# Performance work log

Measured on AMD Instinct MI355X. Metric: run time of the kernel, lower is better.

The kernel has to match this reference:

```python
import jax, jax.numpy as jnp
import numpy as np

B, L, D_MODEL, H = 2, 2048, 1024, 16
D_HEAD = D_MODEL // H
NEG = -1e9


def setup_inputs() -> dict:
    key = jax.random.key(0)
    ks = jax.random.split(key, 8)
    q = jax.random.normal(ks[0], (B, L, D_MODEL), dtype=jnp.float32)
    k = jax.random.normal(ks[1], (B, L, D_MODEL), dtype=jnp.float32)
    v = jax.random.normal(ks[2], (B, L, D_MODEL), dtype=jnp.float32)
    # causal mask: True where attention is disallowed (masked_fill semantics)
    mask = jnp.broadcast_to(jnp.triu(jnp.ones((L, L), dtype=bool), k=1), (B, L, L))
    s = 1.0 / np.sqrt(D_MODEL)
    Wq = jax.random.normal(ks[3], (D_MODEL, D_MODEL), dtype=jnp.float32) * s
    Wk = jax.random.normal(ks[4], (D_MODEL, D_MODEL), dtype=jnp.float32) * s
    Wv = jax.random.normal(ks[5], (D_MODEL, D_MODEL), dtype=jnp.float32) * s
    Wo = jax.random.normal(ks[6], (D_MODEL, D_MODEL), dtype=jnp.float32) * s
    return {"q": q, "k": k, "v": v, "mask": mask,
            "Wq": Wq, "Wk": Wk, "Wv": Wv, "Wo": Wo}


def reference(q, k, v, mask, Wq, Wk, Wv, Wo):
    # projections (Linear, bias=False)
    qh = (q @ Wq).reshape(B, L, H, D_HEAD)
    kh = (k @ Wk).reshape(B, L, H, D_HEAD)
    vh = (v @ Wv).reshape(B, L, H, D_HEAD)
    # per-head scores: contiguous d_model slices == head reshape
    scores = jnp.einsum("bqhd,bkhd->bhqk", qh, kh)
    scores = jnp.where(mask[:, None, :, :], NEG, scores)
    # NOTE: original applies softmax FIRST, then divides by sqrt(d_head)
    weights = jax.nn.softmax(scores, axis=-1) / np.sqrt(D_HEAD).astype(np.float32)
    att = jnp.einsum("bhqk,bkhd->bqhd", weights, vh).reshape(B, L, D_MODEL)
    # dropout is identity in eval mode
    return att @ Wo
```

## Files before the change

kernel.cpp:

```cpp
#include <hip/hip_runtime.h>
#include <hip/hip_bf16.h>

#define BATCH  2
#define SEQ    2048
#define DMODEL 1024
#define NHEAD  16
#define DHEAD  64

typedef _Float16 f16x4 __attribute__((ext_vector_type(4)));
typedef _Float16 f16x8 __attribute__((ext_vector_type(8)));
typedef float    f32x4 __attribute__((ext_vector_type(4)));

union H16 { unsigned short u; _Float16 f; };
__device__ __forceinline__ _Float16 u2h(unsigned short u) { H16 c; c.u = u; return c.f; }
__device__ __forceinline__ unsigned short h2u(_Float16 f) { H16 c; c.f = f; return c.u; }

__device__ __forceinline__ void gll16(const void* g, void* l) {
    __builtin_amdgcn_global_load_lds(
        (const __attribute__((address_space(1))) void*)g,
        (__attribute__((address_space(3))) void*)l, 16, 0, 0);
}

__device__ __forceinline__ void pack_body(const float* __restrict__ W,
                                          _Float16* __restrict__ Phi,
                                          _Float16* __restrict__ Plo)
{
    const int n0 = blockIdx.x * 64;
    const int k0 = blockIdx.y * 64;
    const int t  = threadIdx.x;
    const int nl = t & 63;
    const int kc = (t >> 6) * 16;
    const int n  = n0 + nl;
    const int sw = (n & 3) ^ ((n >> 2) & 3);

    _Float16 hi[16], lo[16];
#pragma unroll
    for (int i = 0; i < 16; i++) {
        float x = W[(size_t)(k0 + kc + i) * DMODEL + n] * 32.0f;
        _Float16 h = (_Float16)x;
        hi[i] = h;
        lo[i] = (_Float16)(x - (float)h);
    }
#pragma unroll
    for (int cc = 0; cc < 2; cc++) {
        const int kk = kc + cc * 8;
        const int g  = kk >> 5;
        const int c  = (kk >> 3) & 3;
        const size_t off = (size_t)n * DMODEL + k0 + g * 32 + ((c ^ sw) << 3);
        *(f16x8*)&Phi[off] = *(f16x8*)&hi[cc * 8];
        if (Plo) *(f16x8*)&Plo[off] = *(f16x8*)&lo[cc * 8];
    }
}

__global__ __launch_bounds__(256) void pack_qkv(const float* __restrict__ Wq,
                                                const float* __restrict__ Wk,
                                                const float* __restrict__ Wv,
                                                _Float16* qhiT, _Float16* qloT,
                                                _Float16* khiT, _Float16* kloT,
                                                _Float16* vhiT)
{
    const int z = blockIdx.z;
    pack_body(z == 0 ? Wq : z == 1 ? Wk : Wv,
              z == 0 ? qhiT : z == 1 ? khiT : vhiT,
              z == 0 ? qloT : z == 1 ? kloT : nullptr);
}

__global__ __launch_bounds__(256) void pack_one(const float* __restrict__ W,
                                                _Float16* Phi)
{
    pack_body(W, Phi, nullptr);
}

template <int SPLIT, typename CT>
__global__ __launch_bounds__(256) void gemm_mfma(const float* __restrict__ A0,
                                                 const float* __restrict__ A1,
                                                 const _Float16* __restrict__ Bh0,
                                                 const _Float16* __restrict__ Bl0,
                                                 const _Float16* __restrict__ Bh1,
                                                 const _Float16* __restrict__ Bl1,
                                                 CT* __restrict__ C0,
                                                 CT* __restrict__ C1,
                                                 int N, int K)
{
    constexpr int ASZ = 128 * 40;
    constexpr int BSZ = 128 * 32;
    constexpr int AHI = 0;
    constexpr int ALO = ASZ;
    constexpr int BHI = ASZ * (SPLIT == 3 ? 2 : 1);
    constexpr int BLO = BHI + 2 * BSZ;
    constexpr int TOT = BHI + 2 * BSZ * (SPLIT == 3 ? 2 : 1);
    __shared__ __align__(16) _Float16 smem[TOT];

    const float*    A  = blockIdx.z ? A1 : A0;
    const _Float16* Bh = blockIdx.z ? Bh1 : Bh0;
    const _Float16* Bl = blockIdx.z ? Bl1 : Bl0;
    CT*             C  = blockIdx.z ? C1 : C0;

    const int m0 = blockIdx.x * 128;
    const int n0 = blockIdx.y * 128;
    const int t    = threadIdx.x;
    const int wave = t >> 6;
    const int lane = t & 63;
    const int quad = lane >> 4;
    const int col  = lane & 15;
    const int wm   = (wave & 1) * 64;
    const int wn   = (wave >> 1) * 64;

    const int ar  = t >> 1;
    const int akc = (t & 1) * 16;
    const float* Ap = A + (size_t)(m0 + ar) * K + akc;

    const _Float16* BhSrc = Bh + (size_t)(n0 + wave * 32 + (lane >> 2)) * K + (lane & 3) * 8;
    const _Float16* BlSrc = (SPLIT == 3)
        ? Bl + (size_t)(n0 + wave * 32 + (lane >> 2)) * K + (lane & 3) * 8 : nullptr;

    const int qe8 = (quad ^ ((col & 3) ^ ((col >> 2) & 3))) * 8;

    f32x4 acc[4][4];
#pragma unroll
    for (int mt = 0; mt < 4; mt++)
#pragma unroll
        for (int nt = 0; nt < 4; nt++) acc[mt][nt] = (f32x4){0.f, 0.f, 0.f, 0.f};

    float av[16];
    auto loadA = [&](int k0) {
#pragma unroll
        for (int g = 0; g < 4; g++) {
            float4 x = *(const float4*)(Ap + k0 + g * 4);
            av[g * 4 + 0] = x.x; av[g * 4 + 1] = x.y;
            av[g * 4 + 2] = x.z; av[g * 4 + 3] = x.w;
        }
    };
    auto issueB = [&](int k0, int buf) {
        _Float16* d0 = &smem[BHI + buf * BSZ + wave * 1024];
        gll16(BhSrc + k0, d0);
        gll16(BhSrc + (size_t)16 * K + k0, d0 + 512);
        if constexpr (SPLIT == 3) {
            _Float16* d1 = &smem[BLO + buf * BSZ + wave * 1024];
            gll16(BlSrc + k0, d1);
            gll16(BlSrc + (size_t)16 * K + k0, d1 + 512);
        }
    };
    auto storeA = [&]() {
#pragma unroll
        for (int g = 0; g < 2; g++) {
            f16x8 h, l;
#pragma unroll
            for (int j = 0; j < 8; j++) {
                float x = av[g * 8 + j];
                _Float16 hh = (_Float16)x;
                h[j] = hh;
                l[j] = (_Float16)(x - (float)hh);
            }
            *(f16x8*)&smem[AHI + ar * 40 + akc + g * 8] = h;
            if constexpr (SPLIT == 3)
                *(f16x8*)&smem[ALO + ar * 40 + akc + g * 8] = l;
        }
    };

    loadA(0);
    issueB(0, 0);

    int buf = 0;
    for (int k0 = 0; k0 < K; k0 += 32, buf ^= 1) {
        storeA();
        __syncthreads();

        if (k0 + 32 < K) { issueB(k0 + 32, buf ^ 1); loadA(k0 + 32); }

        f16x8 ah[4], al[4], bh[4], bl[4];
#pragma unroll
        for (int mt = 0; mt < 4; mt++) {
            ah[mt] = *(f16x8*)&smem[AHI + (wm + mt * 16 + col) * 40 + quad * 8];
            if constexpr (SPLIT == 3)
                al[mt] = *(f16x8*)&smem[ALO + (wm + mt * 16 + col) * 40 + quad * 8];
        }
#pragma unroll
        for (int nt = 0; nt < 4; nt++) {
            bh[nt] = *(f16x8*)&smem[BHI + buf * BSZ + (wn + nt * 16 + col) * 32 + qe8];
            if constexpr (SPLIT == 3)
                bl[nt] = *(f16x8*)&smem[BLO + buf * BSZ + (wn + nt * 16 + col) * 32 + qe8];
        }
#pragma unroll
        for (int nt = 0; nt < 4; nt++)
#pragma unroll
            for (int mt = 0; mt < 4; mt++) {
                acc[mt][nt] = __builtin_amdgcn_mfma_f32_16x16x32_f16(ah[mt], bh[nt], acc[mt][nt], 0, 0, 0);
                if constexpr (SPLIT == 3) {
                    acc[mt][nt] = __builtin_amdgcn_mfma_f32_16x16x32_f16(ah[mt], bl[nt], acc[mt][nt], 0, 0, 0);
                    acc[mt][nt] = __builtin_amdgcn_mfma_f32_16x16x32_f16(al[mt], bh[nt], acc[mt][nt], 0, 0, 0);
                }
            }
        __syncthreads();
    }

    const float inv = 1.0f / 32.0f;
#pragma unroll
    for (int mt = 0; mt < 4; mt++)
#pragma unroll
        for (int nt = 0; nt < 4; nt++)
#pragma unroll
            for (int r = 0; r < 4; r++) {
                float val = acc[mt][nt][r] * inv;
                size_t idx = (size_t)(m0 + wm + mt * 16 + quad * 4 + r) * N
                           + n0 + wn + nt * 16 + col;
                if constexpr (SPLIT == 3) {
                    _Float16 h = (_Float16)val;
                    _Float16 l = (_Float16)(val - (float)h);
                    C[idx] = (unsigned)h2u(h) | ((unsigned)h2u(l) << 16);
                } else if constexpr (__is_same(CT, _Float16)) {
                    C[idx] = (_Float16)val;
                } else {
                    C[idx] = val;
                }
            }
}

#define LDS_STRIDE 72
#define KHI_OFF 0
#define KLO_OFF (64 * LDS_STRIDE)
#define VT_OFF  (2 * 64 * LDS_STRIDE)
#define VT_SIZE (64 * LDS_STRIDE + 64)
#define P_OFF   (VT_OFF + VT_SIZE)
#define P_WAVE  (16 * LDS_STRIDE)
#define SMEM_HALVES (P_OFF + 4 * P_WAVE)

__global__ __launch_bounds__(256) void attn_mfma(unsigned* __restrict__ qa,
                                                 const unsigned* __restrict__ kh,
                                                 const _Float16* __restrict__ vh)
{
    __shared__ __align__(16) _Float16 smem[SMEM_HALVES];

    const int i  = blockIdx.x;
    const int j  = i >> 3;
    const int bh = (i & 7) + ((j & 3) << 3);
    const int qt = (SEQ / 64 - 1) - (j >> 2);
    const int b  = bh >> 4;
    const int h  = bh & 15;
    const int qb = qt * 64;

    const int t    = threadIdx.x;
    const int wave = t >> 6;
    const int lane = t & 63;
    const int quad = lane >> 4;
    const int col  = lane & 15;

    const size_t bbase = (size_t)b * SEQ * DMODEL + (size_t)h * DHEAD;
    const unsigned* kb_ptr = kh + bbase;
    const _Float16* vb_ptr = vh + bbase;

    const int qm = qb + wave * 16 + col;
    f16x8 qhi[2], qlo[2];
    {
        const unsigned* qp = qa + bbase + (size_t)qm * DMODEL + quad * 8;
#pragma unroll
        for (int kt = 0; kt < 2; kt++) {
            uint4 u0 = *(const uint4*)(qp + kt * 32);
            uint4 u1 = *(const uint4*)(qp + kt * 32 + 4);
            unsigned us[8] = {u0.x, u0.y, u0.z, u0.w, u1.x, u1.y, u1.z, u1.w};
#pragma unroll
            for (int jj = 0; jj < 8; jj++) {
                qhi[kt][jj] = u2h((unsigned short)(us[jj] & 0xffffu));
                qlo[kt][jj] = u2h((unsigned short)(us[jj] >> 16));
            }
        }
    }

    const int srow = t >> 2;
    const int sdg  = (t & 3) << 4;
    const int vswz = (t & 3) * 16;

    f16x8 kOnes;
#pragma unroll
    for (int jj = 0; jj < 8; jj++) kOnes[jj] = (_Float16)1.0f;

    float m_i[4];
    f32x4 l4 = (f32x4){0.f, 0.f, 0.f, 0.f};
    f32x4 o[4];
#pragma unroll
    for (int r = 0; r < 4; r++) m_i[r] = -1e30f;
#pragma unroll
    for (int dt = 0; dt < 4; dt++) o[dt] = (f32x4){0.f, 0.f, 0.f, 0.f};

    const int wq0 = qb + wave * 16;
    _Float16* Pw = &smem[P_OFF + wave * P_WAVE];

    f16x8 pkhi[2], pklo[2], pv[2];
    auto load_tile = [&](int kb) {
        const unsigned* kp = kb_ptr + (size_t)(kb + srow) * DMODEL + sdg;
        uint4 u0 = *(const uint4*)(kp + 0);
        uint4 u1 = *(const uint4*)(kp + 4);
        uint4 u2 = *(const uint4*)(kp + 8);
        uint4 u3 = *(const uint4*)(kp + 12);
        unsigned us[16] = {u0.x, u0.y, u0.z, u0.w, u1.x, u1.y, u1.z, u1.w,
                           u2.x, u2.y, u2.z, u2.w, u3.x, u3.y, u3.z, u3.w};
#pragma unroll
        for (int g = 0; g < 2; g++)
#pragma unroll
            for (int jj = 0; jj < 8; jj++) {
                pkhi[g][jj] = u2h((unsigned short)(us[g * 8 + jj] & 0xffffu));
                pklo[g][jj] = u2h((unsigned short)(us[g * 8 + jj] >> 16));
            }
        const _Float16* vp = vb_ptr + (size_t)(kb + srow) * DMODEL + sdg;
        pv[0] = *(const f16x8*)vp;
        pv[1] = *(const f16x8*)(vp + 8);
    };

    load_tile(0);

    for (int kb = 0; kb <= qb; kb += 64) {
        __syncthreads();

        *(f16x8*)&smem[KHI_OFF + srow * LDS_STRIDE + sdg]     = pkhi[0];
        *(f16x8*)&smem[KHI_OFF + srow * LDS_STRIDE + sdg + 8] = pkhi[1];
        *(f16x8*)&smem[KLO_OFF + srow * LDS_STRIDE + sdg]     = pklo[0];
        *(f16x8*)&smem[KLO_OFF + srow * LDS_STRIDE + sdg + 8] = pklo[1];
#pragma unroll
        for (int jj = 0; jj < 8; jj++) {
            smem[VT_OFF + (sdg + jj    ) * LDS_STRIDE + vswz + srow] = pv[0][jj];
            smem[VT_OFF + (sdg + 8 + jj) * LDS_STRIDE + vswz + srow] = pv[1][jj];
        }
        __syncthreads();

        if (kb + 64 <= qb) load_tile(kb + 64);

        if (kb > wq0 + 15) continue;

        f32x4 acc[4];
#pragma unroll
        for (int ct = 0; ct < 4; ct++) acc[ct] = (f32x4){0.f, 0.f, 0.f, 0.f};
#pragma unroll
        for (int kt = 0; kt < 2; kt++) {
#pragma unroll
            for (int ct = 0; ct < 4; ct++) {
                f16x8 bhi = *(f16x8*)&smem[KHI_OFF + (ct * 16 + col) * LDS_STRIDE + kt * 32 + quad * 8];
                f16x8 blo = *(f16x8*)&smem[KLO_OFF + (ct * 16 + col) * LDS_STRIDE + kt * 32 + quad * 8];
                acc[ct] = __builtin_amdgcn_mfma_f32_16x16x32_f16(qhi[kt], bhi, acc[ct], 0, 0, 0);
                acc[ct] = __builtin_amdgcn_mfma_f32_16x16x32_f16(qhi[kt], blo, acc[ct], 0, 0, 0);
                acc[ct] = __builtin_amdgcn_mfma_f32_16x16x32_f16(qlo[kt], bhi, acc[ct], 0, 0, 0);
            }
        }

        const bool need_mask = (kb + 63 > wq0);
#pragma unroll
        for (int r = 0; r < 4; r++) {
            const int qrow = wq0 + quad * 4 + r;
            float s0 = acc[0][r], s1 = acc[1][r], s2 = acc[2][r], s3 = acc[3][r];
            if (need_mask) {
                s0 = (kb +  0 + col <= qrow) ? s0 : -1e30f;
                s1 = (kb + 16 + col <= qrow) ? s1 : -1e30f;
                s2 = (kb + 32 + col <= qrow) ? s2 : -1e30f;
                s3 = (kb + 48 + col <= qrow) ? s3 : -1e30f;
            }
            float rm = fmaxf(fmaxf(s0, s1), fmaxf(s2, s3));
#pragma unroll
            for (int off = 1; off <= 8; off <<= 1)
                rm = fmaxf(rm, __shfl_xor(rm, off, 64));
            const float mnew  = fmaxf(m_i[r], rm);
            const float alpha = __expf(m_i[r] - mnew);
            const float p0 = __expf(s0 - mnew), p1 = __expf(s1 - mnew);
            const float p2 = __expf(s2 - mnew), p3 = __expf(s3 - mnew);
            m_i[r] = mnew;
            l4[r] *= alpha;
#pragma unroll
            for (int dt = 0; dt < 4; dt++) o[dt][r] *= alpha;
            const int prow = quad * 4 + r;
            Pw[prow * LDS_STRIDE + col     ] = (_Float16)p0;
            Pw[prow * LDS_STRIDE + col + 16] = (_Float16)p1;
            Pw[prow * LDS_STRIDE + col + 32] = (_Float16)p2;
            Pw[prow * LDS_STRIDE + col + 48] = (_Float16)p3;
        }

#pragma unroll
        for (int kt = 0; kt < 2; kt++) {
            f16x8 a = *(f16x8*)&Pw[col * LDS_STRIDE + kt * 32 + quad * 8];
            l4 = __builtin_amdgcn_mfma_f32_16x16x32_f16(a, kOnes, l4, 0, 0, 0);
#pragma unroll
            for (int dt = 0; dt < 4; dt++) {
                f16x8 bv = *(f16x8*)&smem[VT_OFF + (dt * 16 + col) * LDS_STRIDE + (dt & 3) * 16 + kt * 32 + quad * 8];
                o[dt] = __builtin_amdgcn_mfma_f32_16x16x32_f16(a, bv, o[dt], 0, 0, 0);
            }
        }
    }

#pragma unroll
    for (int r = 0; r < 4; r++) {
        const float inv = 1.0f / (l4[r] * 8.0f);
        const int q = wq0 + quad * 4 + r;
        unsigned* op = qa + bbase + (size_t)q * DMODEL;
#pragma unroll
        for (int dt = 0; dt < 4; dt++)
            op[dt * 16 + col] = __float_as_uint(o[dt][r] * inv);
    }
}

extern "C" void kernel_launch(void* const* d_in, const int* in_sizes, int n_in,
                              void* d_out, int out_size, void* d_ws, size_t ws_size,
                              hipStream_t stream)
{
    const float* q  = (const float*)d_in[0];
    const float* k  = (const float*)d_in[1];
    const float* v  = (const float*)d_in[2];
    const float* Wq = (const float*)d_in[4];
    const float* Wk = (const float*)d_in[5];
    const float* Wv = (const float*)d_in[6];
    const float* Wo = (const float*)d_in[7];
    float* out = (float*)d_out;

    const int    M   = BATCH * SEQ;
    const size_t npe = (size_t)M * DMODEL;
    const size_t PW  = (size_t)DMODEL * DMODEL;

    unsigned* qh = (unsigned*)d_ws;
    unsigned* kh = qh + npe;

    _Float16* dh    = (_Float16*)d_out;
    _Float16* qhiT  = dh;
    _Float16* qloT  = dh + PW;
    _Float16* khiT  = dh + 2 * PW;
    _Float16* kloT  = dh + 3 * PW;
    _Float16* vhiT  = dh + 4 * PW;
    _Float16* vh    = dh;
    _Float16* wohiT = (_Float16*)kh;

    dim3 b256(256);
    dim3 pk(DMODEL / 64, DMODEL / 64, 3);
    dim3 pk1(DMODEL / 64, DMODEL / 64, 1);
    dim3 gqk(M / 128, DMODEL / 128, 2);
    dim3 g1(M / 128, DMODEL / 128, 1);
    dim3 agrid(1024);

    pack_qkv<<<pk, b256, 0, stream>>>(Wq, Wk, Wv, qhiT, qloT, khiT, kloT, vhiT);
    gemm_mfma<3, unsigned><<<gqk, b256, 0, stream>>>(q, k, qhiT, qloT, khiT, kloT,
                                                     qh, kh, DMODEL, DMODEL);
    gemm_mfma<1, _Float16><<<g1, b256, 0, stream>>>(v, v, vhiT, nullptr, vhiT, nullptr,
                                                    vh, vh, DMODEL, DMODEL);
    attn_mfma<<<agrid, b256, 0, stream>>>(qh, kh, vh);
    pack_one<<<pk1, b256, 0, stream>>>(Wo, wohiT);
    gemm_mfma<1, float><<<g1, b256, 0, stream>>>((const float*)qh, (const float*)qh,
                                                 wohiT, nullptr, wohiT, nullptr,
                                                 out, out, DMODEL, DMODEL);
}
```

Measured before the change: 352.5 us.

## Store K as separate hi/lo planes and double-buffer them into LDS via direct loads

The QK projection GEMM now writes K as two separate fp16 planes (hi and lo) instead of packed 32-bit pairs. The attention kernel then streams K tiles straight into swizzled, double-buffered LDS using global_load_lds, instead of staging through registers and unpacking. This removes the register unpack and the LDS store traffic for K, and lets the next K tile load overlap the current compute. The row-max reduction also switches from shuffles to DPP, and the early skip for fully masked waves is dropped, which adds some redundant work on diagonal tiles.

After: 334.3 us. 1.05x faster.

```diff
diff --git a/kernel.cpp b/kernel.cpp
--- a/kernel.cpp
+++ b/kernel.cpp
@@ -19,6 +19,19 @@
     __builtin_amdgcn_global_load_lds(
         (const __attribute__((address_space(1))) void*)g,
         (__attribute__((address_space(3))) void*)l, 16, 0, 0);
+}
+
+__device__ __forceinline__ float dpp_max16(float x) {
+    float t;
+    t = __int_as_float(__builtin_amdgcn_update_dpp(0, __float_as_int(x), 0xB1, 0xF, 0xF, true));
+    x = fmaxf(x, t);
+    t = __int_as_float(__builtin_amdgcn_update_dpp(0, __float_as_int(x), 0x4E, 0xF, 0xF, true));
+    x = fmaxf(x, t);
+    t = __int_as_float(__builtin_amdgcn_update_dpp(0, __float_as_int(x), 0x124, 0xF, 0xF, true));
+    x = fmaxf(x, t);
+    t = __int_as_float(__builtin_amdgcn_update_dpp(0, __float_as_int(x), 0x128, 0xF, 0xF, true));
+    x = fmaxf(x, t);
+    return x;
 }
 
 __device__ __forceinline__ void pack_body(const float* __restrict__ W,
@@ -80,6 +93,8 @@
                                                  const _Float16* __restrict__ Bl1,
                                                  CT* __restrict__ C0,
                                                  CT* __restrict__ C1,
+                                                 _Float16* __restrict__ Kh,
+                                                 _Float16* __restrict__ Kl,
                                                  int N, int K)
 {
     constexpr int ASZ = 128 * 40;
@@ -206,8 +221,13 @@
                            + n0 + wn + nt * 16 + col;
                 if constexpr (SPLIT == 3) {
                     _Float16 h = (_Float16)val;
-                    _Float16 l = (_Float16)(val - (float)h);
-                    C[idx] = (unsigned)h2u(h) | ((unsigned)h2u(l) << 16);
+                    if (blockIdx.z == 0) {
+                        _Float16 l = (_Float16)(val - (float)h);
+                        C[idx] = (unsigned)h2u(h) | ((unsigned)h2u(l) << 16);
+                    } else {
+                        Kh[idx] = h;
+                        Kl[idx] = (_Float16)(val - (float)h);
+                    }
                 } else if constexpr (__is_same(CT, _Float16)) {
                     C[idx] = (_Float16)val;
                 } else {
@@ -216,20 +236,20 @@
             }
 }
 
-#define LDS_STRIDE 72
-#define KHI_OFF 0
-#define KLO_OFF (64 * LDS_STRIDE)
-#define VT_OFF  (2 * 64 * LDS_STRIDE)
-#define VT_SIZE (64 * LDS_STRIDE + 64)
-#define P_OFF   (VT_OFF + VT_SIZE)
-#define P_WAVE  (16 * LDS_STRIDE)
-#define SMEM_HALVES (P_OFF + 4 * P_WAVE)
+#define AKH 0
+#define AKL 8192
+#define AVT 16384
+#define AVT_SIZE (64 * 72 + 64)
+#define AP  (AVT + AVT_SIZE)
+#define AP_WAVE (16 * 72)
+#define ATOT (AP + 4 * AP_WAVE)
 
 __global__ __launch_bounds__(256) void attn_mfma(unsigned* __restrict__ qa,
-                                                 const unsigned* __restrict__ kh,
+                                                 const _Float16* __restrict__ khi,
+                                                 const _Float16* __restrict__ klo,
                                                  const _Float16* __restrict__ vh)
 {
-    __shared__ __align__(16) _Float16 smem[SMEM_HALVES];
+    __shared__ __align__(16) _Float16 smem[ATOT];
 
     const int i  = blockIdx.x;
     const int j  = i >> 3;
@@ -246,7 +266,6 @@
     const int col  = lane & 15;
 
     const size_t bbase = (size_t)b * SEQ * DMODEL + (size_t)h * DHEAD;
-    const unsigned* kb_ptr = kh + bbase;
     const _Float16* vb_ptr = vh + bbase;
 
     const int qm = qb + wave * 16 + col;
@@ -266,65 +285,62 @@
         }
     }
 
+    const int rl0  = wave * 16 + (lane >> 3);
+    const int kswz = (lane & 7) ^ ((lane >> 3) & 7);
+    const size_t kbase = ((size_t)b * SEQ + rl0) * DMODEL + h * DHEAD + (kswz << 3);
+
+    auto issueK = [&](int kb, int buf) {
+        const _Float16* sh = khi + kbase + (size_t)kb * DMODEL;
+        const _Float16* sl = klo + kbase + (size_t)kb * DMODEL;
+        _Float16* dh = &smem[AKH + buf * 4096 + wave * 1024];
+        _Float16* dl = &smem[AKL + buf * 4096 + wave * 1024];
+        gll16(sh, dh);
+        gll16(sh + (size_t)8 * DMODEL, dh + 512);
+        gll16(sl, dl);
+        gll16(sl + (size_t)8 * DMODEL, dl + 512);
+    };
+
     const int srow = t >> 2;
     const int sdg  = (t & 3) << 4;
     const int vswz = (t & 3) * 16;
-
-    f16x8 kOnes;
-#pragma unroll
-    for (int jj = 0; jj < 8; jj++) kOnes[jj] = (_Float16)1.0f;
-
-    float m_i[4];
-    f32x4 l4 = (f32x4){0.f, 0.f, 0.f, 0.f};
-    f32x4 o[4];
-#pragma unroll
-    for (int r = 0; r < 4; r++) m_i[r] = -1e30f;
-#pragma unroll
-    for (int dt = 0; dt < 4; dt++) o[dt] = (f32x4){0.f, 0.f, 0.f, 0.f};
-
-    const int wq0 = qb + wave * 16;
-    _Float16* Pw = &smem[P_OFF + wave * P_WAVE];
-
-    f16x8 pkhi[2], pklo[2], pv[2];
-    auto load_tile = [&](int kb) {
-        const unsigned* kp = kb_ptr + (size_t)(kb + srow) * DMODEL + sdg;
-        uint4 u0 = *(const uint4*)(kp + 0);
-        uint4 u1 = *(const uint4*)(kp + 4);
-        uint4 u2 = *(const uint4*)(kp + 8);
-        uint4 u3 = *(const uint4*)(kp + 12);
-        unsigned us[16] = {u0.x, u0.y, u0.z, u0.w, u1.x, u1.y, u1.z, u1.w,
-                           u2.x, u2.y, u2.z, u2.w, u3.x, u3.y, u3.z, u3.w};
-#pragma unroll
-        for (int g = 0; g < 2; g++)
-#pragma unroll
-            for (int jj = 0; jj < 8; jj++) {
-                pkhi[g][jj] = u2h((unsigned short)(us[g * 8 + jj] & 0xffffu));
-                pklo[g][jj] = u2h((unsigned short)(us[g * 8 + jj] >> 16));
-            }
+    f16x8 pv[2];
+    auto loadV = [&](int kb) {
         const _Float16* vp = vb_ptr + (size_t)(kb + srow) * DMODEL + sdg;
         pv[0] = *(const f16x8*)vp;
         pv[1] = *(const f16x8*)(vp + 8);
     };
 
-    load_tile(0);
-
-    for (int kb = 0; kb <= qb; kb += 64) {
+    f16x8 kOnes;
+#pragma unroll
+    for (int jj = 0; jj < 8; jj++) kOnes[jj] = (_Float16)1.0f;
+
+    float m_i[4];
+    f32x4 l4 = (f32x4){0.f, 0.f, 0.f, 0.f};
+    f32x4 o[4];
+#pragma unroll
+    for (int r = 0; r < 4; r++) m_i[r] = -1e30f;
+#pragma unroll
+    for (int dt = 0; dt < 4; dt++) o[dt] = (f32x4){0.f, 0.f, 0.f, 0.f};
+
+    const int wq0 = qb + wave * 16;
+    _Float16* Pw = &smem[AP + wave * AP_WAVE];
+    const int cs = col & 7;
+
+    loadV(0);
+    issueK(0, 0);
+
+    int buf = 0;
+    for (int kb = 0; kb <= qb; kb += 64, buf ^= 1) {
         __syncthreads();
 
-        *(f16x8*)&smem[KHI_OFF + srow * LDS_STRIDE + sdg]     = pkhi[0];
-        *(f16x8*)&smem[KHI_OFF + srow * LDS_STRIDE + sdg + 8] = pkhi[1];
-        *(f16x8*)&smem[KLO_OFF + srow * LDS_STRIDE + sdg]     = pklo[0];
-        *(f16x8*)&smem[KLO_OFF + srow * LDS_STRIDE + sdg + 8] = pklo[1];
 #pragma unroll
         for (int jj = 0; jj < 8; jj++) {
-            smem[VT_OFF + (sdg + jj    ) * LDS_STRIDE + vswz + srow] = pv[0][jj];
-            smem[VT_OFF + (sdg + 8 + jj) * LDS_STRIDE + vswz + srow] = pv[1][jj];
+            smem[AVT + (sdg + jj    ) * 72 + vswz + srow] = pv[0][jj];
+            smem[AVT + (sdg + 8 + jj) * 72 + vswz + srow] = pv[1][jj];
         }
         __syncthreads();
 
-        if (kb + 64 <= qb) load_tile(kb + 64);
-
-        if (kb > wq0 + 15) continue;
+        if (kb + 64 <= qb) { issueK(kb + 64, buf ^ 1); loadV(kb + 64); }
 
         f32x4 acc[4];
 #pragma unroll
@@ -333,8 +349,9 @@
         for (int kt = 0; kt < 2; kt++) {
 #pragma unroll
             for (int ct = 0; ct < 4; ct++) {
-                f16x8 bhi = *(f16x8*)&smem[KHI_OFF + (ct * 16 + col) * LDS_STRIDE + kt * 32 + quad * 8];
-                f16x8 blo = *(f16x8*)&smem[KLO_OFF + (ct * 16 + col) * LDS_STRIDE + kt * 32 + quad * 8];
+                const int off = (ct * 16 + col) * 64 + ((((kt << 2) | quad) ^ cs) << 3);
+                f16x8 bhi = *(f16x8*)&smem[AKH + buf * 4096 + off];
+                f16x8 blo = *(f16x8*)&smem[AKL + buf * 4096 + off];
                 acc[ct] = __builtin_amdgcn_mfma_f32_16x16x32_f16(qhi[kt], bhi, acc[ct], 0, 0, 0);
                 acc[ct] = __builtin_amdgcn_mfma_f32_16x16x32_f16(qhi[kt], blo, acc[ct], 0, 0, 0);
                 acc[ct] = __builtin_amdgcn_mfma_f32_16x16x32_f16(qlo[kt], bhi, acc[ct], 0, 0, 0);
@@ -352,10 +369,7 @@
                 s2 = (kb + 32 + col <= qrow) ? s2 : -1e30f;
                 s3 = (kb + 48 + col <= qrow) ? s3 : -1e30f;
             }
-            float rm = fmaxf(fmaxf(s0, s1), fmaxf(s2, s3));
-#pragma unroll
-            for (int off = 1; off <= 8; off <<= 1)
-                rm = fmaxf(rm, __shfl_xor(rm, off, 64));
+            float rm = dpp_max16(fmaxf(fmaxf(s0, s1), fmaxf(s2, s3)));
             const float mnew  = fmaxf(m_i[r], rm);
             const float alpha = __expf(m_i[r] - mnew);
             const float p0 = __expf(s0 - mnew), p1 = __expf(s1 - mnew);
@@ -365,19 +379,19 @@
 #pragma unroll
             for (int dt = 0; dt < 4; dt++) o[dt][r] *= alpha;
             const int prow = quad * 4 + r;
-            Pw[prow * LDS_STRIDE + col     ] = (_Float16)p0;
-            Pw[prow * LDS_STRIDE + col + 16] = (_Float16)p1;
-            Pw[prow * LDS_STRIDE + col + 32] = (_Float16)p2;
-            Pw[prow * LDS_STRIDE + col + 48] = (_Float16)p3;
+            Pw[prow * 72 + col     ] = (_Float16)p0;
+            Pw[prow * 72 + col + 16] = (_Float16)p1;
+            Pw[prow * 72 + col + 32] = (_Float16)p2;
+            Pw[prow * 72 + col + 48] = (_Float16)p3;
         }
 
 #pragma unroll
         for (int kt = 0; kt < 2; kt++) {
-            f16x8 a = *(f16x8*)&Pw[col * LDS_STRIDE + kt * 32 + quad * 8];
+            f16x8 a = *(f16x8*)&Pw[col * 72 + kt * 32 + quad * 8];
             l4 = __builtin_amdgcn_mfma_f32_16x16x32_f16(a, kOnes, l4, 0, 0, 0);
 #pragma unroll
             for (int dt = 0; dt < 4; dt++) {
-                f16x8 bv = *(f16x8*)&smem[VT_OFF + (dt * 16 + col) * LDS_STRIDE + (dt & 3) * 16 + kt * 32 + quad * 8];
+                f16x8 bv = *(f16x8*)&smem[AVT + (dt * 16 + col) * 72 + (dt & 3) * 16 + kt * 32 + quad * 8];
                 o[dt] = __builtin_amdgcn_mfma_f32_16x16x32_f16(a, bv, o[dt], 0, 0, 0);
             }
         }
@@ -411,8 +425,9 @@
     const size_t npe = (size_t)M * DMODEL;
     const size_t PW  = (size_t)DMODEL * DMODEL;
 
-    unsigned* qh = (unsigned*)d_ws;
-    unsigned* kh = qh + npe;
+    unsigned* qh    = (unsigned*)d_ws;
+    _Float16* khi_p = (_Float16*)(qh + npe);
+    _Float16* klo_p = khi_p + npe;
 
     _Float16* dh    = (_Float16*)d_out;
     _Float16* qhiT  = dh;
@@ -421,7 +436,7 @@
     _Float16* kloT  = dh + 3 * PW;
     _Float16* vhiT  = dh + 4 * PW;
     _Float16* vh    = dh;
-    _Float16* wohiT = (_Float16*)kh;
+    _Float16* wohiT = khi_p;
 
     dim3 b256(256);
     dim3 pk(DMODEL / 64, DMODEL / 64, 3);
@@ -432,12 +447,15 @@
 
     pack_qkv<<<pk, b256, 0, stream>>>(Wq, Wk, Wv, qhiT, qloT, khiT, kloT, vhiT);
     gemm_mfma<3, unsigned><<<gqk, b256, 0, stream>>>(q, k, qhiT, qloT, khiT, kloT,
-                                                     qh, kh, DMODEL, DMODEL);
+                                                     qh, nullptr, khi_p, klo_p,
+                                                     DMODEL, DMODEL);
     gemm_mfma<1, _Float16><<<g1, b256, 0, stream>>>(v, v, vhiT, nullptr, vhiT, nullptr,
-                                                    vh, vh, DMODEL, DMODEL);
-    attn_mfma<<<agrid, b256, 0, stream>>>(qh, kh, vh);
+                                                    vh, vh, nullptr, nullptr,
+                                                    DMODEL, DMODEL);
+    attn_mfma<<<agrid, b256, 0, stream>>>(qh, khi_p, klo_p, vh);
     pack_one<<<pk1, b256, 0, stream>>>(Wo, wohiT);
     gemm_mfma<1, float><<<g1, b256, 0, stream>>>((const float*)qh, (const float*)qh,
                                                  wohiT, nullptr, wohiT, nullptr,
-                                                 out, out, DMODEL, DMODEL);
-}
+                                                 out, out, nullptr, nullptr,
+                                                 DMODEL, DMODEL);
+}
```
